# Kernel optimization log

Measured on AMD Instinct MI355X. Metric: run time of the kernel, lower is better.

The kernel has to match this reference:

```python
import jax, jax.numpy as jnp
import numpy as np

KS = 3  # deformable kernel size
PAD = 1


def conv2d(x, w, b=None, stride=1, pad=1):
    out = jax.lax.conv_general_dilated(
        x, w, (stride, stride), [(pad, pad), (pad, pad)],
        dimension_numbers=('NCHW', 'OIHW', 'NCHW'))
    if b is not None:
        out = out + b[None, :, None, None]
    return out


def group_norm(x, gamma, beta, groups, eps=1e-5):
    b, c, h, w = x.shape
    xg = x.reshape(b, groups, c // groups, h, w)
    mu = jnp.mean(xg, axis=(2, 3, 4), keepdims=True)
    var = jnp.mean((xg - mu) ** 2, axis=(2, 3, 4), keepdims=True)
    xn = ((xg - mu) / jnp.sqrt(var + eps)).reshape(b, c, h, w)
    return xn * gamma[None, :, None, None] + beta[None, :, None, None]


def deform_conv2d(x, w_p, b_p, w_m, b_m, w_main):
    # Faithful port of the pure-PyTorch DeformConv2d (modulation=True, k=3, pad=1, stride=1).
    ks, pad = KS, PAD
    N = ks * ks
    offset = conv2d(x, w_p, b_p, 1, 1)             # (b, 2N, h, w)
    m = jax.nn.sigmoid(conv2d(x, w_m, b_m, 1, 1))  # (b, N, h, w) modulation mask
    b_, c, h, w = x.shape
    xp = jnp.pad(x, ((0, 0), (0, 0), (pad, pad), (pad, pad)))  # zero padding before sampling
    Hp, Wp = h + 2 * pad, w + 2 * pad
    r = (ks - 1) // 2
    pi, pj = jnp.meshgrid(jnp.arange(-r, r + 1), jnp.arange(-r, r + 1), indexing='ij')
    p_n = jnp.concatenate([pi.reshape(-1), pj.reshape(-1)]).astype(x.dtype)  # (2N,)
    gi, gj = jnp.meshgrid(jnp.arange(1, h + 1), jnp.arange(1, w + 1), indexing='ij')
    p0 = jnp.concatenate([jnp.tile(gi[None], (N, 1, 1)),
                          jnp.tile(gj[None], (N, 1, 1))], 0).astype(x.dtype)  # (2N, h, w)
    p = offset + p_n[None, :, None, None] + p0[None]  # (b, 2N, h, w) sample coords in padded frame
    p = jnp.transpose(p, (0, 2, 3, 1))                # (b, h, w, 2N)
    px, py = p[..., :N], p[..., N:]
    fx, fy = jnp.floor(px), jnp.floor(py)
    q_lt_x = jnp.clip(fx, 0, Hp - 1).astype(jnp.int32)
    q_lt_y = jnp.clip(fy, 0, Wp - 1).astype(jnp.int32)
    q_rb_x = jnp.clip(fx + 1, 0, Hp - 1).astype(jnp.int32)
    q_rb_y = jnp.clip(fy + 1, 0, Wp - 1).astype(jnp.int32)
    px = jnp.clip(px, 0, Hp - 1)
    py = jnp.clip(py, 0, Wp - 1)
    g_lt = (1 + (q_lt_x - px)) * (1 + (q_lt_y - py))
    g_rb = (1 - (q_rb_x - px)) * (1 - (q_rb_y - py))
    g_lb = (1 + (q_lt_x - px)) * (1 - (q_rb_y - py))
    g_rt = (1 - (q_rb_x - px)) * (1 + (q_lt_y - py))
    xf = xp.reshape(b_, c, Hp * Wp)

    def gather(qx, qy):
        idx = (qx * Wp + qy).reshape(b_, 1, -1)  # (b, 1, h*w*N)
        out = jnp.take_along_axis(xf, jnp.broadcast_to(idx, (b_, c, idx.shape[-1])), axis=2)
        return out.reshape(b_, c, h, w, N)

    x_off = (g_lt[:, None] * gather(q_lt_x, q_lt_y)
             + g_rb[:, None] * gather(q_rb_x, q_rb_y)
             + g_lb[:, None] * gather(q_lt_x, q_rb_y)
             + g_rt[:, None] * gather(q_rb_x, q_lt_y))  # (b, c, h, w, N)
    x_off = x_off * jnp.transpose(m, (0, 2, 3, 1))[:, None]  # apply modulation
    # N is ordered (ki outer, kj inner); tile to (b, c, h*ks, w*ks) and conv with stride=ks
    x_off = x_off.reshape(b_, c, h, w, ks, ks).transpose(0, 1, 2, 4, 3, 5).reshape(b_, c, h * ks, w * ks)
    return conv2d(x_off, w_main, None, stride=ks, pad=0)  # main conv has no bias


def dsa_forward(x, wp1, bp1, wm1, bm1, wc1, g1, be1, wa, ba, wb, bb,
                wp2, bp2, wm2, bm2, wc2, g2, be2):
    C = x.shape[1]
    c1 = jax.nn.relu(group_norm(deform_conv2d(x, wp1, bp1, wm1, bm1, wc1), g1, be1, C // 4))
    avg = jax.nn.sigmoid(conv2d(jnp.mean(c1, axis=1, keepdims=True), wa, ba))  # (b,1,h,w)
    mx = jax.nn.sigmoid(conv2d(jnp.max(c1, axis=1, keepdims=True), wb, bb))    # (b,1,h,w)
    out = jnp.concatenate([avg * c1, mx * c1], axis=1)  # (b, 2C, h, w)
    return jax.nn.relu(group_norm(deform_conv2d(out, wp2, bp2, wm2, bm2, wc2), g2, be2, C // 4))


def setup_inputs() -> dict:
    key = jax.random.key(0)
    ks = jax.random.split(key, 10)
    B, C, H, W = 2, 64, 128, 128
    N = 9

    def nrm(k, shape, s=1.0):
        return jax.random.normal(k, shape, dtype=jnp.float32) * s

    return dict(
        x=nrm(ks[0], (B, C, H, W)),
        wp1=nrm(ks[1], (2 * N, C, 3, 3), 0.01), bp1=jnp.zeros((2 * N,), jnp.float32),
        wm1=nrm(ks[2], (N, C, 3, 3), 0.05), bm1=jnp.zeros((N,), jnp.float32),
        wc1=nrm(ks[3], (C, C, 3, 3), 0.05),
        g1=jnp.ones((C,), jnp.float32), be1=jnp.zeros((C,), jnp.float32),
        wa=nrm(ks[4], (1, 1, 3, 3), 0.3), ba=jnp.zeros((1,), jnp.float32),
        wb=nrm(ks[5], (1, 1, 3, 3), 0.3), bb=jnp.zeros((1,), jnp.float32),
        wp2=nrm(ks[6], (2 * N, 2 * C, 3, 3), 0.01), bp2=jnp.zeros((2 * N,), jnp.float32),
        wm2=nrm(ks[7], (N, 2 * C, 3, 3), 0.05), bm2=jnp.zeros((N,), jnp.float32),
        wc2=nrm(ks[8], (C, 2 * C, 3, 3), 0.03),
        g2=jnp.ones((C,), jnp.float32), be2=jnp.zeros((C,), jnp.float32),
    )


def reference(x, wp1, bp1, wm1, bm1, wc1, g1, be1, wa, ba, wb, bb,
              wp2, bp2, wm2, bm2, wc2, g2, be2):
    return dsa_forward(x, wp1, bp1, wm1, bm1, wc1, g1, be1, wa, ba, wb, bb,
                       wp2, bp2, wm2, bm2, wc2, g2, be2)
```

## Files before the change

kernel.cpp:

```cpp
#include <hip/hip_runtime.h>
#include <hip/hip_bf16.h>
#include <math.h>

#define H 128
#define W 128
#define HW (H*W)
#define BATCH 2

typedef __attribute__((ext_vector_type(8))) short          bf16x8;
typedef __attribute__((ext_vector_type(4))) float          f32x4;
typedef __attribute__((ext_vector_type(8))) unsigned short u16x8;

__device__ __forceinline__ float sigmoidf_(float x){ return 1.0f/(1.0f + expf(-x)); }

__device__ __forceinline__ unsigned short f2bf(float f) {
    __hip_bfloat16 h = __float2bfloat16(f);
    return __builtin_bit_cast(unsigned short, h);
}
__device__ __forceinline__ float bf2f(unsigned short b) {
    return __uint_as_float(((unsigned)b) << 16);
}
__device__ __forceinline__ float bflo(unsigned u){ return __uint_as_float(u << 16); }
__device__ __forceinline__ float bfhi(unsigned u){ return __uint_as_float(u & 0xFFFF0000u); }

__global__ __launch_bounds__(256) void prep_all(
    const float* __restrict__ x,
    const float* __restrict__ wc1, const float* __restrict__ wc2,
    const float* __restrict__ wp1, const float* __restrict__ wm1,
    const float* __restrict__ wp2, const float* __restrict__ wm2,
    unsigned short* __restrict__ xt,
    unsigned short* __restrict__ wtp1, unsigned short* __restrict__ wtp2,
    unsigned short* __restrict__ wop1, unsigned short* __restrict__ wop2,
    float* __restrict__ stats1, float* __restrict__ stats2)
{
    __shared__ float tile[64][65];
    if (blockIdx.x < 512) {
        if (blockIdx.x == 0 && threadIdx.x < 128) {
            if (threadIdx.x < 64) stats1[threadIdx.x] = 0.f;
            else                  stats2[threadIdx.x - 64] = 0.f;
        }
        int blk = blockIdx.x;
        int b  = blk >> 8;
        int p0 = (blk & 255) * 64;
        int tr = threadIdx.x >> 6;
        int tc = threadIdx.x & 63;
        #pragma unroll
        for (int r = 0; r < 16; r++) {
            int c = r * 4 + tr;
            tile[c][tc] = x[((size_t)b * 64 + c) * HW + p0 + tc];
        }
        __syncthreads();
        #pragma unroll
        for (int r = 0; r < 16; r++) {
            int p = r * 4 + tr;
            xt[((size_t)b * HW + p0 + p) * 64 + tc] = f2bf(tile[tc][p]);
        }
        return;
    }
    const int s1 = 64 * 9 * 64, s2 = 64 * 9 * 128;
    const int s3 = 32 * 9 * 64, s4 = 32 * 9 * 128;
    int t = (blockIdx.x - 512) * 256 + threadIdx.x;
    if (t < s1) {
        int oc = t / (9 * 64); int r = t - oc * (9 * 64);
        int n = r / 64, c = r - n * 64;
        wtp1[t] = f2bf(wc1[((size_t)oc * 64 + c) * 9 + n]);
        return;
    }
    t -= s1;
    if (t < s2) {
        int oc = t / (9 * 128); int r = t - oc * (9 * 128);
        int n = r / 128, c = r - n * 128;
        wtp2[t] = f2bf(wc2[((size_t)oc * 128 + c) * 9 + n]);
        return;
    }
    t -= s2;
    if (t < s3) {
        int oc = t / (9 * 64); int r = t - oc * (9 * 64);
        int n = r / 64, c = r - n * 64;
        float v = 0.f;
        if (oc < 18)      v = wp1[((size_t)oc * 64 + c) * 9 + n];
        else if (oc < 27) v = wm1[((size_t)(oc - 18) * 64 + c) * 9 + n];
        wop1[t] = f2bf(v);
        return;
    }
    t -= s3;
    if (t < s4) {
        int oc = t / (9 * 128); int r = t - oc * (9 * 128);
        int n = r / 128, c = r - n * 128;
        float v = 0.f;
        if (oc < 18)      v = wp2[((size_t)oc * 128 + c) * 9 + n];
        else if (oc < 27) v = wm2[((size_t)(oc - 18) * 128 + c) * 9 + n];
        wop2[t] = f2bf(v);
    }
}

template<int CIN>
__global__ __launch_bounds__(512, 6) void dsa_fused(
    const unsigned short* __restrict__ xt,
    const unsigned short* __restrict__ wop,
    const unsigned short* __restrict__ wtp,
    const float* __restrict__ bp,
    const float* __restrict__ bm,
    float* __restrict__ out,
    float* __restrict__ stats)
{
    constexpr int HPC  = CIN / 64;
    constexpr int NCH  = 9 * HPC;
    constexpr int SROW = 68;
    __shared__ __align__(16) unsigned short sbuf[2][64][SROW];
    __shared__ __align__(16) unsigned short wbuf[2][64][SROW];
    __shared__ __align__(16) unsigned short meta[9][64][8];
    __shared__ float offlds[27][68];
    __shared__ float wsp[8][8][2];

    int tid  = threadIdx.x;
    int bid  = blockIdx.x;
    int wgid = (bid & 7) * 64 + (bid >> 3);
    int pix0 = wgid * 64;
    int b    = pix0 >> 14;
    int base = pix0 & (HW - 1);
    int i    = base >> 7;
    int j0   = base & 127;

    const unsigned short* xtb = xt + (size_t)b * HW * CIN;
    const u16x8 zero8 = {0,0,0,0,0,0,0,0};

    int lane = tid & 63, wv = tid >> 6;
    int lr = lane & 15, lg = lane >> 4;

    {
        auto sample = [&](int cc, int bi) {
            int n = cc / HPC, h = cc - n * HPC;
            int di = n / 3 - 1, dj = n - (n / 3) * 3 - 1;
            int ii = i + di;
            bool rowok = (ii >= 0 && ii < H);
            int p = tid >> 3, cl = tid & 7;
            int jj = j0 + p + dj;
            bool v = rowok && (jj >= 0 && jj < W);
            u16x8 val = v ? *reinterpret_cast<const u16x8*>(
                                xtb + (size_t)(ii * W + jj) * CIN + h * 64 + cl * 8)
                          : zero8;
            *reinterpret_cast<u16x8*>(&sbuf[bi][p][cl * 8]) = val;
        };
        auto stage_w = [&](int cc, int bi) {
            if (tid < 256) {
                int n = cc / HPC, h = cc - n * HPC;
                int row = tid >> 3, seg = tid & 7;
                u16x8 v = *reinterpret_cast<const u16x8*>(
                    wop + (size_t)row * (9 * CIN) + n * CIN + h * 64 + seg * 8);
                *reinterpret_cast<u16x8*>(&wbuf[bi][row][seg * 8]) = v;
            }
        };

        sample(0, 0);
        stage_w(0, 0);
        __syncthreads();

        int mt = wv & 1, nt = wv >> 1;
        int srow = nt * 16 + lr;
        int wrow = mt * 16 + lr;
        f32x4 acc = {0.f, 0.f, 0.f, 0.f};

        for (int cc = 0; cc < NCH; cc++) {
            int cur = cc & 1;
            #pragma unroll
            for (int ks = 0; ks < 2; ks++) {
                bf16x8 bfr = *reinterpret_cast<const bf16x8*>(&sbuf[cur][srow][ks * 32 + lg * 8]);
                bf16x8 a   = *reinterpret_cast<const bf16x8*>(&wbuf[cur][wrow][ks * 32 + lg * 8]);
                acc = __builtin_amdgcn_mfma_f32_16x16x32_bf16(a, bfr, acc, 0, 0, 0);
            }
            if (cc + 1 < NCH) {
                sample(cc + 1, cur ^ 1);
                stage_w(cc + 1, cur ^ 1);
            }
            __syncthreads();
        }

        int plocal = nt * 16 + lr;
        #pragma unroll
        for (int r = 0; r < 4; r++) {
            int oc = mt * 16 + lg * 4 + r;
            if (oc < 27) {
                float v = acc[r];
                v = (oc < 18) ? (v + bp[oc]) : sigmoidf_(v + bm[oc - 18]);
                offlds[oc][plocal] = v;
            }
        }
    }
    __syncthreads();

    for (int task = tid; task < 576; task += 512) {
        int p = task & 63, n = task >> 6;
        int j = j0 + p;
        float px = offlds[n][p]      + (float)(n / 3 - 1) + (float)(i + 1);
        float py = offlds[9 + n][p]  + (float)(n % 3 - 1) + (float)(j + 1);
        float mk = offlds[18 + n][p];
        float fx = floorf(px), fy = floorf(py);
        const float lim = 129.0f;
        int qltx = (int)fminf(fmaxf(fx, 0.f), lim);
        int qlty = (int)fminf(fmaxf(fy, 0.f), lim);
        int qrbx = (int)fminf(fmaxf(fx + 1.f, 0.f), lim);
        int qrby = (int)fminf(fmaxf(fy + 1.f, 0.f), lim);
        float pxc = fminf(fmaxf(px, 0.f), lim);
        float pyc = fminf(fmaxf(py, 0.f), lim);
        float gxl = 1.f + ((float)qltx - pxc);
        float gxr = 1.f - ((float)qrbx - pxc);
        float gyl = 1.f + ((float)qlty - pyc);
        float gyr = 1.f - ((float)qrby - pyc);
        int   xs[4] = {qltx, qrbx, qltx, qrbx};
        int   ys[4] = {qlty, qrby, qrby, qlty};
        float gs[4] = {gxl * gyl, gxr * gyr, gxl * gyr, gxr * gyl};
        u16x8 m;
        #pragma unroll
        for (int q = 0; q < 4; q++) {
            int qx = xs[q], qy = ys[q];
            bool valid = (qx >= 1 && qx <= H && qy >= 1 && qy <= W);
            m[q]     = valid ? (unsigned short)((qx - 1) * W + (qy - 1)) : (unsigned short)0;
            m[4 + q] = f2bf(valid ? gs[q] * mk : 0.f);
        }
        *reinterpret_cast<u16x8*>(&meta[n][p][0]) = m;
    }
    __syncthreads();

    {
        auto sample = [&](int cc, int bi) {
            int n = cc / HPC, h = cc - n * HPC;
            int p = tid >> 3, cl = tid & 7;
            u16x8 m = *reinterpret_cast<const u16x8*>(&meta[n][p][0]);
            float vac[8];
            #pragma unroll
            for (int e = 0; e < 8; e++) vac[e] = 0.f;
            #pragma unroll
            for (int q = 0; q < 4; q++) {
                const unsigned short* sp = xtb + (size_t)m[q] * CIN + h * 64 + cl * 8;
                u16x8 v = *reinterpret_cast<const u16x8*>(sp);
                float wq = bf2f(m[4 + q]);
                const unsigned* vd = reinterpret_cast<const unsigned*>(&v);
                #pragma unroll
                for (int d = 0; d < 4; d++) {
                    vac[2 * d]     = fmaf(bflo(vd[d]), wq, vac[2 * d]);
                    vac[2 * d + 1] = fmaf(bfhi(vd[d]), wq, vac[2 * d + 1]);
                }
            }
            u16x8 o;
            #pragma unroll
            for (int e = 0; e < 8; e++) o[e] = f2bf(vac[e]);
            *reinterpret_cast<u16x8*>(&sbuf[bi][p][cl * 8]) = o;
        };
        auto stage_w = [&](int cc, int bi) {
            int n = cc / HPC, h = cc - n * HPC;
            int row = tid >> 3, seg = tid & 7;
            u16x8 v = *reinterpret_cast<const u16x8*>(
                wtp + (size_t)row * (9 * CIN) + n * CIN + h * 64 + seg * 8);
            *reinterpret_cast<u16x8*>(&wbuf[bi][row][seg * 8]) = v;
        };

        sample(0, 0);
        stage_w(0, 0);
        __syncthreads();

        int ocq = wv & 1, pq = wv >> 1;
        int srow = pq * 16 + lr;
        int wrow = ocq * 32 + lr;

        f32x4 acc0 = {0.f, 0.f, 0.f, 0.f};
        f32x4 acc1 = {0.f, 0.f, 0.f, 0.f};

        for (int cc = 0; cc < NCH; cc++) {
            int cur = cc & 1;
            #pragma unroll
            for (int ks = 0; ks < 2; ks++) {
                bf16x8 bfr = *reinterpret_cast<const bf16x8*>(&sbuf[cur][srow][ks * 32 + lg * 8]);
                bf16x8 a0  = *reinterpret_cast<const bf16x8*>(&wbuf[cur][wrow][ks * 32 + lg * 8]);
                bf16x8 a1  = *reinterpret_cast<const bf16x8*>(&wbuf[cur][wrow + 16][ks * 32 + lg * 8]);
                acc0 = __builtin_amdgcn_mfma_f32_16x16x32_bf16(a0, bfr, acc0, 0, 0, 0);
                acc1 = __builtin_amdgcn_mfma_f32_16x16x32_bf16(a1, bfr, acc1, 0, 0, 0);
            }
            if (cc + 1 < NCH) {
                sample(cc + 1, cur ^ 1);
                stage_w(cc + 1, cur ^ 1);
            }
            __syncthreads();
        }

        int pixo = base + pq * 16 + lr;
        float* ob0 = out + ((size_t)b * 64 + ocq * 32 + lg * 4) * HW + pixo;
        #pragma unroll
        for (int r = 0; r < 4; r++) ob0[(size_t)r * HW] = acc0[r];
        float* ob1 = out + ((size_t)b * 64 + ocq * 32 + 16 + lg * 4) * HW + pixo;
        #pragma unroll
        for (int r = 0; r < 4; r++) ob1[(size_t)r * HW] = acc1[r];

        float s0 = 0.f, q0 = 0.f, s1 = 0.f, q1 = 0.f;
        #pragma unroll
        for (int r = 0; r < 4; r++) {
            s0 += acc0[r]; q0 += acc0[r] * acc0[r];
            s1 += acc1[r]; q1 += acc1[r] * acc1[r];
        }
        #pragma unroll
        for (int d = 1; d < 16; d <<= 1) {
            s0 += __shfl_xor(s0, d); q0 += __shfl_xor(q0, d);
            s1 += __shfl_xor(s1, d); q1 += __shfl_xor(q1, d);
        }
        if (lr == 0) {
            wsp[wv][lg][0]     = s0; wsp[wv][lg][1]     = q0;
            wsp[wv][4 + lg][0] = s1; wsp[wv][4 + lg][1] = q1;
        }
        __syncthreads();
        if (tid < 16) {
            int g = tid, par = g >> 3, e = g & 7;
            float ss = 0.f, qq = 0.f;
            #pragma unroll
            for (int w = 0; w < 4; w++) {
                ss += wsp[par + 2 * w][e][0];
                qq += wsp[par + 2 * w][e][1];
            }
            atomicAdd(&stats[b * 16 + g], ss);
            atomicAdd(&stats[32 + b * 16 + g], qq);
        }
    }
}

__global__ __launch_bounds__(256) void attn_cat_t(
    const float* __restrict__ dc, const float* __restrict__ stats,
    const float* __restrict__ gamma, const float* __restrict__ beta,
    const float* __restrict__ wa, const float* __restrict__ ba,
    const float* __restrict__ wb, const float* __restrict__ bb,
    unsigned short* __restrict__ catt)
{
    __shared__ float tile[64][65];
    __shared__ float cm_l[3][66], cx_l[3][66];
    __shared__ float avs[64], mvs[64];
    __shared__ float mg[16], rg[16], gam[64], bet[64];
    int blk = blockIdx.x;
    int b  = blk >> 8;
    int p0 = (blk & 255) * 64;
    int i  = p0 >> 7;
    int j0 = p0 & 127;
    int tx = threadIdx.x;

    if (tx < 16) {
        float s = stats[b * 16 + tx], q = stats[32 + b * 16 + tx];
        float mean = s * (1.0f / (4.0f * HW));
        float var  = q * (1.0f / (4.0f * HW)) - mean * mean;
        mg[tx] = mean; rg[tx] = rsqrtf(var + 1e-5f);
    }
    if (tx < 64) { gam[tx] = gamma[tx]; bet[tx] = beta[tx]; }
    __syncthreads();

    if (tx < 198) {
        int hr = tx / 66, hc = tx - hr * 66;
        int ii = i + hr - 1, jj = j0 + hc - 1;
        float msum = 0.f, mmax = 0.f;
        if (ii >= 0 && ii < H && jj >= 0 && jj < W) {
            int pixg = ii * W + jj;
            for (int c = 0; c < 64; c++) {
                float v = dc[((size_t)b * 64 + c) * HW + pixg];
                int g = c >> 2;
                v = fmaxf((v - mg[g]) * rg[g] * gam[c] + bet[c], 0.f);
                msum += v;
                mmax = fmaxf(mmax, v);
            }
            cm_l[hr][hc] = msum * (1.0f / 64.0f);
            cx_l[hr][hc] = mmax;
        } else {
            cm_l[hr][hc] = 0.f;
            cx_l[hr][hc] = 0.f;
        }
    }
    {
        int tr = tx >> 6, tc = tx & 63;
        #pragma unroll
        for (int r = 0; r < 16; r++) {
            int c = r * 4 + tr;
            float v = dc[((size_t)b * 64 + c) * HW + p0 + tc];
            tile[c][tc] = fmaxf((v - mg[c >> 2]) * rg[c >> 2] * gam[c] + bet[c], 0.f);
        }
    }
    __syncthreads();

    if (tx < 64) {
        int p = tx;
        float sa = ba[0], sb = bb[0];
        #pragma unroll
        for (int di = 0; di < 3; di++) {
            #pragma unroll
            for (int dj = 0; dj < 3; dj++) {
                sa = fmaf(cm_l[di][p + dj], wa[di * 3 + dj], sa);
                sb = fmaf(cx_l[di][p + dj], wb[di * 3 + dj], sb);
            }
        }
        avs[p] = sigmoidf_(sa);
        mvs[p] = sigmoidf_(sb);
    }
    __syncthreads();

    {
        int tr = tx >> 6, tc = tx & 63;
        #pragma unroll
        for (int r = 0; r < 16; r++) {
            int p = r * 4 + tr;
            float v = tile[tc][p];
            unsigned short* cr = catt + ((size_t)b * HW + p0 + p) * 128;
            cr[tc]      = f2bf(avs[p] * v);
            cr[64 + tc] = f2bf(mvs[p] * v);
        }
    }
}

__global__ __launch_bounds__(256) void gn_final(
    const float* __restrict__ dc, const float* __restrict__ stats,
    const float* __restrict__ gamma, const float* __restrict__ beta,
    float* __restrict__ out)
{
    int t = blockIdx.x * 256 + threadIdx.x;
    if (t >= BATCH * 64 * HW) return;
    int c = (t >> 14) & 63;
    int b = t >> 20;
    int g = c >> 2;
    float s = stats[b * 16 + g], q = stats[32 + b * 16 + g];
    float mean = s * (1.0f / (4.0f * HW));
    float var  = q * (1.0f / (4.0f * HW)) - mean * mean;
    float rstd = rsqrtf(var + 1e-5f);
    float v = (dc[t] - mean) * rstd * gamma[c] + beta[c];
    out[t] = fmaxf(v, 0.f);
}

extern "C" void kernel_launch(void* const* d_in, const int* in_sizes, int n_in,
                              void* d_out, int out_size, void* d_ws, size_t ws_size,
                              hipStream_t stream) {
    (void)in_sizes; (void)n_in; (void)out_size; (void)ws_size;
    const float* x   = (const float*)d_in[0];
    const float* wp1 = (const float*)d_in[1];
    const float* bp1 = (const float*)d_in[2];
    const float* wm1 = (const float*)d_in[3];
    const float* bm1 = (const float*)d_in[4];
    const float* wc1 = (const float*)d_in[5];
    const float* g1  = (const float*)d_in[6];
    const float* be1 = (const float*)d_in[7];
    const float* wa  = (const float*)d_in[8];
    const float* ba  = (const float*)d_in[9];
    const float* wb  = (const float*)d_in[10];
    const float* bb  = (const float*)d_in[11];
    const float* wp2 = (const float*)d_in[12];
    const float* bp2 = (const float*)d_in[13];
    const float* wm2 = (const float*)d_in[14];
    const float* bm2 = (const float*)d_in[15];
    const float* wc2 = (const float*)d_in[16];
    const float* g2  = (const float*)d_in[17];
    const float* be2 = (const float*)d_in[18];
    float* out = (float*)d_out;

    float* ws   = (float*)d_ws;
    float* dcb  = ws;
    unsigned short* catt = (unsigned short*)(dcb + 2 * 64 * HW);
    float* st1  = (float*)(catt + (size_t)2 * 128 * HW);
    float* st2  = st1 + 64;
    unsigned short* wtp1 = (unsigned short*)(st2 + 64);
    unsigned short* wtp2 = wtp1 + 64 * 576;
    unsigned short* wop1 = wtp2 + 64 * 1152;
    unsigned short* wop2 = wop1 + 32 * 576;
    unsigned short* xt1 = (unsigned short*)out;

    const int NDEF  = BATCH * HW / 64;
    const int NPREP = 512 + (64 * 576 + 64 * 1152 + 32 * 576 + 32 * 1152 + 255) / 256;

    prep_all<<<NPREP, 256, 0, stream>>>(x, wc1, wc2, wp1, wm1, wp2, wm2,
                                        xt1, wtp1, wtp2, wop1, wop2, st1, st2);

    dsa_fused<64><<<NDEF, 512, 0, stream>>>(xt1, wop1, wtp1, bp1, bm1, dcb, st1);
    attn_cat_t<<<512, 256, 0, stream>>>(dcb, st1, g1, be1,
                                        wa, ba, wb, bb, catt);

    dsa_fused<128><<<NDEF, 512, 0, stream>>>(catt, wop2, wtp2, bp2, bm2, dcb, st2);
    gn_final<<<(BATCH * 64 * HW + 255) / 256, 256, 0, stream>>>(dcb, st2, g2, be2, out);
}
```

Before: 95.25 us.

## Halve deformable-conv workgroup tile to 32 pixels with 256 threads

Each fused deformable conv block now handles 32 pixels with 4 waves instead of 64 pixels with 8 waves, doubling the grid size. Shared buffers, the metadata and offset loops, the weight-staging loops and the GroupNorm partial reduction are resized to match. The aim is better load balance and occupancy with smaller LDS per block. The cost is that each block re-stages the full weight tile for half as many pixels, doubling weight traffic per output.

Result: no change. 94.42 us (-0.9%).

```diff
diff --git a/kernel.cpp b/kernel.cpp
--- a/kernel.cpp
+++ b/kernel.cpp
@@ -95,7 +95,7 @@
 }
 
 template<int CIN>
-__global__ __launch_bounds__(512, 6) void dsa_fused(
+__global__ __launch_bounds__(256, 4) void dsa_fused(
     const unsigned short* __restrict__ xt,
     const unsigned short* __restrict__ wop,
     const unsigned short* __restrict__ wtp,
@@ -107,16 +107,16 @@
     constexpr int HPC  = CIN / 64;
     constexpr int NCH  = 9 * HPC;
     constexpr int SROW = 68;
-    __shared__ __align__(16) unsigned short sbuf[2][64][SROW];
+    __shared__ __align__(16) unsigned short sbuf[2][32][SROW];
     __shared__ __align__(16) unsigned short wbuf[2][64][SROW];
-    __shared__ __align__(16) unsigned short meta[9][64][8];
-    __shared__ float offlds[27][68];
-    __shared__ float wsp[8][8][2];
+    __shared__ __align__(16) unsigned short meta[9][32][8];
+    __shared__ float offlds[27][36];
+    __shared__ float wsp[4][8][2];
 
     int tid  = threadIdx.x;
     int bid  = blockIdx.x;
-    int wgid = (bid & 7) * 64 + (bid >> 3);
-    int pix0 = wgid * 64;
+    int wgid = (bid & 7) * 128 + (bid >> 3);
+    int pix0 = wgid * 32;
     int b    = pix0 >> 14;
     int base = pix0 & (HW - 1);
     int i    = base >> 7;
@@ -127,6 +127,7 @@
 
     int lane = tid & 63, wv = tid >> 6;
     int lr = lane & 15, lg = lane >> 4;
+    int sp = tid >> 3, scl = tid & 7;
 
     {
         auto sample = [&](int cc, int bi) {
@@ -134,22 +135,18 @@
             int di = n / 3 - 1, dj = n - (n / 3) * 3 - 1;
             int ii = i + di;
             bool rowok = (ii >= 0 && ii < H);
-            int p = tid >> 3, cl = tid & 7;
-            int jj = j0 + p + dj;
+            int jj = j0 + sp + dj;
             bool v = rowok && (jj >= 0 && jj < W);
             u16x8 val = v ? *reinterpret_cast<const u16x8*>(
-                                xtb + (size_t)(ii * W + jj) * CIN + h * 64 + cl * 8)
+                                xtb + (size_t)(ii * W + jj) * CIN + h * 64 + scl * 8)
                           : zero8;
-            *reinterpret_cast<u16x8*>(&sbuf[bi][p][cl * 8]) = val;
+            *reinterpret_cast<u16x8*>(&sbuf[bi][sp][scl * 8]) = val;
         };
         auto stage_w = [&](int cc, int bi) {
-            if (tid < 256) {
-                int n = cc / HPC, h = cc - n * HPC;
-                int row = tid >> 3, seg = tid & 7;
-                u16x8 v = *reinterpret_cast<const u16x8*>(
-                    wop + (size_t)row * (9 * CIN) + n * CIN + h * 64 + seg * 8);
-                *reinterpret_cast<u16x8*>(&wbuf[bi][row][seg * 8]) = v;
-            }
+            int n = cc / HPC, h = cc - n * HPC;
+            u16x8 v = *reinterpret_cast<const u16x8*>(
+                wop + (size_t)sp * (9 * CIN) + n * CIN + h * 64 + scl * 8);
+            *reinterpret_cast<u16x8*>(&wbuf[bi][sp][scl * 8]) = v;
         };
 
         sample(0, 0);
@@ -189,8 +186,8 @@
     }
     __syncthreads();
 
-    for (int task = tid; task < 576; task += 512) {
-        int p = task & 63, n = task >> 6;
+    for (int task = tid; task < 288; task += 256) {
+        int p = task & 31, n = task >> 5;
         int j = j0 + p;
         float px = offlds[n][p]      + (float)(n / 3 - 1) + (float)(i + 1);
         float py = offlds[9 + n][p]  + (float)(n % 3 - 1) + (float)(j + 1);
@@ -225,15 +222,14 @@
     {
         auto sample = [&](int cc, int bi) {
             int n = cc / HPC, h = cc - n * HPC;
-            int p = tid >> 3, cl = tid & 7;
-            u16x8 m = *reinterpret_cast<const u16x8*>(&meta[n][p][0]);
+            u16x8 m = *reinterpret_cast<const u16x8*>(&meta[n][sp][0]);
             float vac[8];
             #pragma unroll
             for (int e = 0; e < 8; e++) vac[e] = 0.f;
             #pragma unroll
             for (int q = 0; q < 4; q++) {
-                const unsigned short* sp = xtb + (size_t)m[q] * CIN + h * 64 + cl * 8;
-                u16x8 v = *reinterpret_cast<const u16x8*>(sp);
+                const unsigned short* spp = xtb + (size_t)m[q] * CIN + h * 64 + scl * 8;
+                u16x8 v = *reinterpret_cast<const u16x8*>(spp);
                 float wq = bf2f(m[4 + q]);
                 const unsigned* vd = reinterpret_cast<const unsigned*>(&v);
                 #pragma unroll
@@ -245,14 +241,18 @@
             u16x8 o;
             #pragma unroll
             for (int e = 0; e < 8; e++) o[e] = f2bf(vac[e]);
-            *reinterpret_cast<u16x8*>(&sbuf[bi][p][cl * 8]) = o;
+            *reinterpret_cast<u16x8*>(&sbuf[bi][sp][scl * 8]) = o;
         };
         auto stage_w = [&](int cc, int bi) {
             int n = cc / HPC, h = cc - n * HPC;
-            int row = tid >> 3, seg = tid & 7;
-            u16x8 v = *reinterpret_cast<const u16x8*>(
-                wtp + (size_t)row * (9 * CIN) + n * CIN + h * 64 + seg * 8);
-            *reinterpret_cast<u16x8*>(&wbuf[bi][row][seg * 8]) = v;
+            #pragma unroll
+            for (int t2 = 0; t2 < 2; t2++) {
+                int idx = t2 * 256 + tid;
+                int row = idx >> 3, seg = idx & 7;
+                u16x8 v = *reinterpret_cast<const u16x8*>(
+                    wtp + (size_t)row * (9 * CIN) + n * CIN + h * 64 + seg * 8);
+                *reinterpret_cast<u16x8*>(&wbuf[bi][row][seg * 8]) = v;
+            }
         };
 
         sample(0, 0);
@@ -309,12 +309,8 @@
         __syncthreads();
         if (tid < 16) {
             int g = tid, par = g >> 3, e = g & 7;
-            float ss = 0.f, qq = 0.f;
-            #pragma unroll
-            for (int w = 0; w < 4; w++) {
-                ss += wsp[par + 2 * w][e][0];
-                qq += wsp[par + 2 * w][e][1];
-            }
+            float ss = wsp[par][e][0] + wsp[par + 2][e][0];
+            float qq = wsp[par][e][1] + wsp[par + 2][e][1];
             atomicAdd(&stats[b * 16 + g], ss);
             atomicAdd(&stats[32 + b * 16 + g], qq);
         }
@@ -462,16 +458,16 @@
     unsigned short* wop2 = wop1 + 32 * 576;
     unsigned short* xt1 = (unsigned short*)out;
 
-    const int NDEF  = BATCH * HW / 64;
+    const int NDEF  = BATCH * HW / 32;
     const int NPREP = 512 + (64 * 576 + 64 * 1152 + 32 * 576 + 32 * 1152 + 255) / 256;
 
     prep_all<<<NPREP, 256, 0, stream>>>(x, wc1, wc2, wp1, wm1, wp2, wm2,
                                         xt1, wtp1, wtp2, wop1, wop2, st1, st2);
 
-    dsa_fused<64><<<NDEF, 512, 0, stream>>>(xt1, wop1, wtp1, bp1, bm1, dcb, st1);
+    dsa_fused<64><<<NDEF, 256, 0, stream>>>(xt1, wop1, wtp1, bp1, bm1, dcb, st1);
     attn_cat_t<<<512, 256, 0, stream>>>(dcb, st1, g1, be1,
                                         wa, ba, wb, bb, catt);
 
-    dsa_fused<128><<<NDEF, 512, 0, stream>>>(catt, wop2, wtp2, bp2, bm2, dcb, st2);
+    dsa_fused<128><<<NDEF, 256, 0, stream>>>(catt, wop2, wtp2, bp2, bm2, dcb, st2);
     gn_final<<<(BATCH * 64 * HW + 255) / 256, 256, 0, stream>>>(dcb, st2, g2, be2, out);
 }
```

## Load MFMA operands directly from global memory, removing LDS staging and barriers

Applied to the files above, without the earlier changes.

Rewrites both GEMM phases of the fused deformable kernel so each wave loads its bilinear-sampled activations and weight fragments straight from global memory into MFMA operand registers. The double-buffered LDS tiles for samples and weights and the per-chunk __syncthreads go away. Block size drops from 512 to 256 threads, so each wave computes 16 pixels across all output channels. This removes LDS traffic and barrier stalls, but weights are now re-read from global or L2 by every wave, gather latency is no longer overlapped by explicit prefetch, and register pressure per thread rises.

Result: slower. 173.1 us (+81.8%).

```diff
diff --git a/kernel.cpp b/kernel.cpp
--- a/kernel.cpp
+++ b/kernel.cpp
@@ -95,7 +95,7 @@
 }
 
 template<int CIN>
-__global__ __launch_bounds__(512, 6) void dsa_fused(
+__global__ __launch_bounds__(256, 4) void dsa_fused(
     const unsigned short* __restrict__ xt,
     const unsigned short* __restrict__ wop,
     const unsigned short* __restrict__ wtp,
@@ -104,14 +104,11 @@
     float* __restrict__ out,
     float* __restrict__ stats)
 {
-    constexpr int HPC  = CIN / 64;
-    constexpr int NCH  = 9 * HPC;
-    constexpr int SROW = 68;
-    __shared__ __align__(16) unsigned short sbuf[2][64][SROW];
-    __shared__ __align__(16) unsigned short wbuf[2][64][SROW];
+    constexpr int HPC = CIN / 64;
+    constexpr int NCH = 9 * HPC;
     __shared__ __align__(16) unsigned short meta[9][64][8];
     __shared__ float offlds[27][68];
-    __shared__ float wsp[8][8][2];
+    __shared__ float wsp[4][16][2];
 
     int tid  = threadIdx.x;
     int bid  = blockIdx.x;
@@ -127,69 +124,45 @@
 
     int lane = tid & 63, wv = tid >> 6;
     int lr = lane & 15, lg = lane >> 4;
+    int pmy = wv * 16 + lr;
 
     {
-        auto sample = [&](int cc, int bi) {
+        f32x4 oa0 = {0.f,0.f,0.f,0.f}, oa1 = {0.f,0.f,0.f,0.f};
+        const unsigned short* wb0 = wop + (size_t)lr * (9 * CIN) + lg * 8;
+        const unsigned short* wb1 = wb0 + (size_t)16 * (9 * CIN);
+        for (int cc = 0; cc < NCH; cc++) {
             int n = cc / HPC, h = cc - n * HPC;
             int di = n / 3 - 1, dj = n - (n / 3) * 3 - 1;
-            int ii = i + di;
-            bool rowok = (ii >= 0 && ii < H);
-            int p = tid >> 3, cl = tid & 7;
-            int jj = j0 + p + dj;
-            bool v = rowok && (jj >= 0 && jj < W);
-            u16x8 val = v ? *reinterpret_cast<const u16x8*>(
-                                xtb + (size_t)(ii * W + jj) * CIN + h * 64 + cl * 8)
-                          : zero8;
-            *reinterpret_cast<u16x8*>(&sbuf[bi][p][cl * 8]) = val;
-        };
-        auto stage_w = [&](int cc, int bi) {
-            if (tid < 256) {
-                int n = cc / HPC, h = cc - n * HPC;
-                int row = tid >> 3, seg = tid & 7;
-                u16x8 v = *reinterpret_cast<const u16x8*>(
-                    wop + (size_t)row * (9 * CIN) + n * CIN + h * 64 + seg * 8);
-                *reinterpret_cast<u16x8*>(&wbuf[bi][row][seg * 8]) = v;
-            }
-        };
-
-        sample(0, 0);
-        stage_w(0, 0);
-        __syncthreads();
-
-        int mt = wv & 1, nt = wv >> 1;
-        int srow = nt * 16 + lr;
-        int wrow = mt * 16 + lr;
-        f32x4 acc = {0.f, 0.f, 0.f, 0.f};
-
-        for (int cc = 0; cc < NCH; cc++) {
-            int cur = cc & 1;
+            int ii = i + di, jj = j0 + pmy + dj;
+            bool ok = (ii >= 0 && ii < H && jj >= 0 && jj < W);
+            int sidx = ok ? (ii * W + jj) : 0;
+            const unsigned short* sb = xtb + (size_t)sidx * CIN + h * 64 + lg * 8;
+            int wo = n * CIN + h * 64;
             #pragma unroll
             for (int ks = 0; ks < 2; ks++) {
-                bf16x8 bfr = *reinterpret_cast<const bf16x8*>(&sbuf[cur][srow][ks * 32 + lg * 8]);
-                bf16x8 a   = *reinterpret_cast<const bf16x8*>(&wbuf[cur][wrow][ks * 32 + lg * 8]);
-                acc = __builtin_amdgcn_mfma_f32_16x16x32_bf16(a, bfr, acc, 0, 0, 0);
+                u16x8 sv = ok ? *reinterpret_cast<const u16x8*>(sb + ks * 32) : zero8;
+                bf16x8 a0 = *reinterpret_cast<const bf16x8*>(wb0 + wo + ks * 32);
+                bf16x8 a1 = *reinterpret_cast<const bf16x8*>(wb1 + wo + ks * 32);
+                bf16x8 bfr = __builtin_bit_cast(bf16x8, sv);
+                oa0 = __builtin_amdgcn_mfma_f32_16x16x32_bf16(a0, bfr, oa0, 0, 0, 0);
+                oa1 = __builtin_amdgcn_mfma_f32_16x16x32_bf16(a1, bfr, oa1, 0, 0, 0);
             }
-            if (cc + 1 < NCH) {
-                sample(cc + 1, cur ^ 1);
-                stage_w(cc + 1, cur ^ 1);
+        }
+        #pragma unroll
+        for (int r = 0; r < 4; r++) {
+            int oc0 = lg * 4 + r;
+            offlds[oc0][pmy] = oa0[r] + bp[oc0];
+            int oc1 = 16 + lg * 4 + r;
+            if (oc1 < 27) {
+                float v = oa1[r];
+                v = (oc1 < 18) ? (v + bp[oc1]) : sigmoidf_(v + bm[oc1 - 18]);
+                offlds[oc1][pmy] = v;
             }
-            __syncthreads();
-        }
-
-        int plocal = nt * 16 + lr;
-        #pragma unroll
-        for (int r = 0; r < 4; r++) {
-            int oc = mt * 16 + lg * 4 + r;
-            if (oc < 27) {
-                float v = acc[r];
-                v = (oc < 18) ? (v + bp[oc]) : sigmoidf_(v + bm[oc - 18]);
-                offlds[oc][plocal] = v;
-            }
         }
     }
     __syncthreads();
 
-    for (int task = tid; task < 576; task += 512) {
+    for (int task = tid; task < 576; task += 256) {
         int p = task & 63, n = task >> 6;
         int j = j0 + p;
         float px = offlds[n][p]      + (float)(n / 3 - 1) + (float)(i + 1);
@@ -223,100 +196,97 @@
     __syncthreads();
 
     {
-        auto sample = [&](int cc, int bi) {
+        f32x4 ac0 = {0.f,0.f,0.f,0.f}, ac1 = {0.f,0.f,0.f,0.f};
+        f32x4 ac2 = {0.f,0.f,0.f,0.f}, ac3 = {0.f,0.f,0.f,0.f};
+        const unsigned short* wt0 = wtp + (size_t)lr * (9 * CIN) + lg * 8;
+        const unsigned short* wt1 = wt0 + (size_t)16 * (9 * CIN);
+        const unsigned short* wt2 = wt0 + (size_t)32 * (9 * CIN);
+        const unsigned short* wt3 = wt0 + (size_t)48 * (9 * CIN);
+
+        for (int cc = 0; cc < NCH; cc++) {
             int n = cc / HPC, h = cc - n * HPC;
-            int p = tid >> 3, cl = tid & 7;
-            u16x8 m = *reinterpret_cast<const u16x8*>(&meta[n][p][0]);
-            float vac[8];
+            u16x8 gm = *reinterpret_cast<const u16x8*>(&meta[n][pmy][0]);
+            float w0 = bf2f(gm[4]), w1 = bf2f(gm[5]);
+            float w2 = bf2f(gm[6]), w3 = bf2f(gm[7]);
+            int off_k = h * 64 + lg * 8;
+            const unsigned short* g0 = xtb + (size_t)gm[0] * CIN + off_k;
+            const unsigned short* g1 = xtb + (size_t)gm[1] * CIN + off_k;
+            const unsigned short* g2 = xtb + (size_t)gm[2] * CIN + off_k;
+            const unsigned short* g3 = xtb + (size_t)gm[3] * CIN + off_k;
+            int wo = n * CIN + off_k - lg * 8;
             #pragma unroll
-            for (int e = 0; e < 8; e++) vac[e] = 0.f;
-            #pragma unroll
-            for (int q = 0; q < 4; q++) {
-                const unsigned short* sp = xtb + (size_t)m[q] * CIN + h * 64 + cl * 8;
-                u16x8 v = *reinterpret_cast<const u16x8*>(sp);
-                float wq = bf2f(m[4 + q]);
-                const unsigned* vd = reinterpret_cast<const unsigned*>(&v);
+            for (int ks = 0; ks < 2; ks++) {
+                u16x8 v0 = *reinterpret_cast<const u16x8*>(g0 + ks * 32);
+                u16x8 v1 = *reinterpret_cast<const u16x8*>(g1 + ks * 32);
+                u16x8 v2 = *reinterpret_cast<const u16x8*>(g2 + ks * 32);
+                u16x8 v3 = *reinterpret_cast<const u16x8*>(g3 + ks * 32);
+                const unsigned* d0 = reinterpret_cast<const unsigned*>(&v0);
+                const unsigned* d1 = reinterpret_cast<const unsigned*>(&v1);
+                const unsigned* d2 = reinterpret_cast<const unsigned*>(&v2);
+                const unsigned* d3 = reinterpret_cast<const unsigned*>(&v3);
+                u16x8 o;
                 #pragma unroll
                 for (int d = 0; d < 4; d++) {
-                    vac[2 * d]     = fmaf(bflo(vd[d]), wq, vac[2 * d]);
-                    vac[2 * d + 1] = fmaf(bfhi(vd[d]), wq, vac[2 * d + 1]);
+                    float lo = bflo(d0[d]) * w0, hi = bfhi(d0[d]) * w0;
+                    lo = fmaf(bflo(d1[d]), w1, lo); hi = fmaf(bfhi(d1[d]), w1, hi);
+                    lo = fmaf(bflo(d2[d]), w2, lo); hi = fmaf(bfhi(d2[d]), w2, hi);
+                    lo = fmaf(bflo(d3[d]), w3, lo); hi = fmaf(bfhi(d3[d]), w3, hi);
+                    o[2 * d]     = f2bf(lo);
+                    o[2 * d + 1] = f2bf(hi);
                 }
+                bf16x8 bfr = __builtin_bit_cast(bf16x8, o);
+                bf16x8 a0 = *reinterpret_cast<const bf16x8*>(wt0 + wo + ks * 32);
+                bf16x8 a1 = *reinterpret_cast<const bf16x8*>(wt1 + wo + ks * 32);
+                bf16x8 a2 = *reinterpret_cast<const bf16x8*>(wt2 + wo + ks * 32);
+                bf16x8 a3 = *reinterpret_cast<const bf16x8*>(wt3 + wo + ks * 32);
+                ac0 = __builtin_amdgcn_mfma_f32_16x16x32_bf16(a0, bfr, ac0, 0, 0, 0);
+                ac1 = __builtin_amdgcn_mfma_f32_16x16x32_bf16(a1, bfr, ac1, 0, 0, 0);
+                ac2 = __builtin_amdgcn_mfma_f32_16x16x32_bf16(a2, bfr, ac2, 0, 0, 0);
+                ac3 = __builtin_amdgcn_mfma_f32_16x16x32_bf16(a3, bfr, ac3, 0, 0, 0);
             }
-            u16x8 o;
-            #pragma unroll
-            for (int e = 0; e < 8; e++) o[e] = f2bf(vac[e]);
-            *reinterpret_cast<u16x8*>(&sbuf[bi][p][cl * 8]) = o;
-        };
-        auto stage_w = [&](int cc, int bi) {
-            int n = cc / HPC, h = cc - n * HPC;
-            int row = tid >> 3, seg = tid & 7;
-            u16x8 v = *reinterpret_cast<const u16x8*>(
-                wtp + (size_t)row * (9 * CIN) + n * CIN + h * 64 + seg * 8);
-            *reinterpret_cast<u16x8*>(&wbuf[bi][row][seg * 8]) = v;
-        };
-
-        sample(0, 0);
-        stage_w(0, 0);
-        __syncthreads();
-
-        int ocq = wv & 1, pq = wv >> 1;
-        int srow = pq * 16 + lr;
-        int wrow = ocq * 32 + lr;
-
-        f32x4 acc0 = {0.f, 0.f, 0.f, 0.f};
-        f32x4 acc1 = {0.f, 0.f, 0.f, 0.f};
-
-        for (int cc = 0; cc < NCH; cc++) {
-            int cur = cc & 1;
-            #pragma unroll
-            for (int ks = 0; ks < 2; ks++) {
-                bf16x8 bfr = *reinterpret_cast<const bf16x8*>(&sbuf[cur][srow][ks * 32 + lg * 8]);
-                bf16x8 a0  = *reinterpret_cast<const bf16x8*>(&wbuf[cur][wrow][ks * 32 + lg * 8]);
-                bf16x8 a1  = *reinterpret_cast<const bf16x8*>(&wbuf[cur][wrow + 16][ks * 32 + lg * 8]);
-                acc0 = __builtin_amdgcn_mfma_f32_16x16x32_bf16(a0, bfr, acc0, 0, 0, 0);
-                acc1 = __builtin_amdgcn_mfma_f32_16x16x32_bf16(a1, bfr, acc1, 0, 0, 0);
-            }
-            if (cc + 1 < NCH) {
-                sample(cc + 1, cur ^ 1);
-                stage_w(cc + 1, cur ^ 1);
-            }
-            __syncthreads();
-        }
-
-        int pixo = base + pq * 16 + lr;
-        float* ob0 = out + ((size_t)b * 64 + ocq * 32 + lg * 4) * HW + pixo;
-        #pragma unroll
-        for (int r = 0; r < 4; r++) ob0[(size_t)r * HW] = acc0[r];
-        float* ob1 = out + ((size_t)b * 64 + ocq * 32 + 16 + lg * 4) * HW + pixo;
-        #pragma unroll
-        for (int r = 0; r < 4; r++) ob1[(size_t)r * HW] = acc1[r];
-
-        float s0 = 0.f, q0 = 0.f, s1 = 0.f, q1 = 0.f;
+        }
+
+        int pixo = base + pmy;
+        float* o0 = out + ((size_t)b * 64 + lg * 4) * HW + pixo;
+        float* o1 = o0 + (size_t)16 * HW;
+        float* o2 = o0 + (size_t)32 * HW;
+        float* o3 = o0 + (size_t)48 * HW;
         #pragma unroll
         for (int r = 0; r < 4; r++) {
-            s0 += acc0[r]; q0 += acc0[r] * acc0[r];
-            s1 += acc1[r]; q1 += acc1[r] * acc1[r];
+            o0[(size_t)r * HW] = ac0[r];
+            o1[(size_t)r * HW] = ac1[r];
+            o2[(size_t)r * HW] = ac2[r];
+            o3[(size_t)r * HW] = ac3[r];
+        }
+
+        float s0 = 0.f, t0 = 0.f, s1 = 0.f, t1 = 0.f;
+        float s2 = 0.f, t2 = 0.f, s3 = 0.f, t3 = 0.f;
+        #pragma unroll
+        for (int r = 0; r < 4; r++) {
+            s0 += ac0[r]; t0 += ac0[r] * ac0[r];
+            s1 += ac1[r]; t1 += ac1[r] * ac1[r];
+            s2 += ac2[r]; t2 += ac2[r] * ac2[r];
+            s3 += ac3[r]; t3 += ac3[r] * ac3[r];
         }
         #pragma unroll
         for (int d = 1; d < 16; d <<= 1) {
-            s0 += __shfl_xor(s0, d); q0 += __shfl_xor(q0, d);
-            s1 += __shfl_xor(s1, d); q1 += __shfl_xor(q1, d);
+            s0 += __shfl_xor(s0, d); t0 += __shfl_xor(t0, d);
+            s1 += __shfl_xor(s1, d); t1 += __shfl_xor(t1, d);
+            s2 += __shfl_xor(s2, d); t2 += __shfl_xor(t2, d);
+            s3 += __shfl_xor(s3, d); t3 += __shfl_xor(t3, d);
         }
         if (lr == 0) {
-            wsp[wv][lg][0]     = s0; wsp[wv][lg][1]     = q0;
-            wsp[wv][4 + lg][0] = s1; wsp[wv][4 + lg][1] = q1;
+            wsp[wv][lg][0]      = s0; wsp[wv][lg][1]      = t0;
+            wsp[wv][4 + lg][0]  = s1; wsp[wv][4 + lg][1]  = t1;
+            wsp[wv][8 + lg][0]  = s2; wsp[wv][8 + lg][1]  = t2;
+            wsp[wv][12 + lg][0] = s3; wsp[wv][12 + lg][1] = t3;
         }
         __syncthreads();
         if (tid < 16) {
-            int g = tid, par = g >> 3, e = g & 7;
-            float ss = 0.f, qq = 0.f;
-            #pragma unroll
-            for (int w = 0; w < 4; w++) {
-                ss += wsp[par + 2 * w][e][0];
-                qq += wsp[par + 2 * w][e][1];
-            }
-            atomicAdd(&stats[b * 16 + g], ss);
-            atomicAdd(&stats[32 + b * 16 + g], qq);
+            float ss = wsp[0][tid][0] + wsp[1][tid][0] + wsp[2][tid][0] + wsp[3][tid][0];
+            float qq = wsp[0][tid][1] + wsp[1][tid][1] + wsp[2][tid][1] + wsp[3][tid][1];
+            atomicAdd(&stats[b * 16 + tid], ss);
+            atomicAdd(&stats[32 + b * 16 + tid], qq);
         }
     }
 }
@@ -468,10 +438,10 @@
     prep_all<<<NPREP, 256, 0, stream>>>(x, wc1, wc2, wp1, wm1, wp2, wm2,
                                         xt1, wtp1, wtp2, wop1, wop2, st1, st2);
 
-    dsa_fused<64><<<NDEF, 512, 0, stream>>>(xt1, wop1, wtp1, bp1, bm1, dcb, st1);
+    dsa_fused<64><<<NDEF, 256, 0, stream>>>(xt1, wop1, wtp1, bp1, bm1, dcb, st1);
     attn_cat_t<<<512, 256, 0, stream>>>(dcb, st1, g1, be1,
                                         wa, ba, wb, bb, catt);
 
-    dsa_fused<128><<<NDEF, 512, 0, stream>>>(catt, wop2, wtp2, bp2, bm2, dcb, st2);
+    dsa_fused<128><<<NDEF, 256, 0, stream>>>(catt, wop2, wtp2, bp2, bm2, dcb, st2);
     gn_final<<<(BATCH * 64 * HW + 255) / 256, 256, 0, stream>>>(dcb, st2, g2, be2, out);
 }
```
